# Performance work log

Measured on AMD Instinct MI355X. Metric: run time of the kernel, lower is better.

## Reference

```python
import jax, jax.numpy as jnp
import numpy as np

L = 7          # window side (odd)
A = 0.3        # weight of average term
B = 0.7        # weight of differential term


def mex_hat(d):
    grid = (np.mgrid[:d, :d] - d // 2) * 1.0
    eucl = np.sqrt((grid ** 2).sum(0)) / d
    return (eucl * np.exp(-eucl)).astype(np.float32)  # (d, d)


def setup_inputs() -> dict:
    key = jax.random.key(0)
    x = jax.random.normal(key, (64, 1, 512, 512), dtype=jnp.float32)
    kernel = jnp.asarray(mex_hat(L).reshape(-1))  # (L*L,), matches unfold row-major order
    return {"x": x, "kernel": kernel}


def reference(x, kernel):
    # x: [B,1,n,n], kernel: [L*L]
    n = x.shape[2]
    pad = L // 2
    xp = jnp.pad(x, ((0, 0), (0, 0), (pad, pad), (pad, pad)))  # zero pad, as F.unfold
    mean_acc = jnp.zeros_like(x)
    diff_acc = jnp.zeros_like(x)
    # fixed 49-offset loop replaces the im2col buffer; each shift is a view-slice
    for i in range(L):
        for j in range(L):
            s = jax.lax.dynamic_slice(xp, (0, 0, i, j), x.shape)
            mean_acc = mean_acc + s
            diff_acc = diff_acc + kernel[i * L + j] * jax.nn.relu(s - x)
    average_term = jnp.exp(-mean_acc / (L * L))              # [B,1,n,n]
    differential_term = diff_acc                             # [B,1,n,n]
    mask = A * average_term + B * differential_term
    mask = mask / jnp.sqrt(jnp.sum(mask ** 2))               # global L2 norm
    out = jnp.where(x > mask, x, jnp.zeros_like(x))
    return out, average_term, differential_term
```

## Files before the change

### kernel.cpp

```cpp
#include <hip/hip_runtime.h>
#include <stdint.h>

#define IMG 512
constexpr int TX = 64, TY = 32, PADW = 3;
constexpr int SMW = TX + 2 * PADW;
constexpr int SMH = TY + 2 * PADW;
constexpr int SMS = SMW + 2;
constexpr int NBX = IMG / TX;
constexpr int NBY = IMG / TY;
constexpr float A_W = 0.3f, B_W = 0.7f;

#define W1  0.12383970f
#define W2  0.16507309f
#define W4  0.21470754f
#define W5  0.23209061f
#define W8  0.26975268f
#define W9  0.27918814f
#define W10 0.28754623f
#define W13 0.30773566f
#define W18 0.33061044f

__device__ constexpr float KW[7][7] = {
    { W18, W13, W10, W9,  W10, W13, W18 },
    { W13, W8,  W5,  W4,  W5,  W8,  W13 },
    { W10, W5,  W2,  W1,  W2,  W5,  W10 },
    { W9,  W4,  W1,  0.f, W1,  W4,  W9  },
    { W10, W5,  W2,  W1,  W2,  W5,  W10 },
    { W13, W8,  W5,  W4,  W5,  W8,  W13 },
    { W18, W13, W10, W9,  W10, W13, W18 },
};

constexpr float ksum_calc() {
    float s = 0.f;
    for (int i = 0; i < 7; ++i)
        for (int j = 0; j < 7; ++j) s += KW[i][j];
    return s;
}
constexpr float KSUM = ksum_calc();

__device__ __forceinline__ void stencil8(const float* __restrict__ sm, int tx, int ty0,
                                         float (&avgO)[8], float (&dO)[8])
{
    float c[8], mean[8], T[8];
    #pragma unroll
    for (int k = 0; k < 8; ++k) {
        c[k] = sm[(ty0 + k + PADW) * SMS + tx + PADW];
        mean[k] = 0.f; T[k] = 0.f;
    }

    #pragma unroll
    for (int wy = 0; wy < 14; ++wy) {
        float s[7];
        const int base = (ty0 + wy) * SMS + tx;
        #pragma unroll
        for (int dx = 0; dx < 7; ++dx) s[dx] = sm[base + dx];
        float rowsum = ((s[0] + s[1]) + (s[2] + s[3])) + ((s[4] + s[5]) + s[6]);
        #pragma unroll
        for (int k = 0; k < 8; ++k) {
            const int dy = wy - k;
            if (dy >= 0 && dy < 7) {
                mean[k] += rowsum;
                #pragma unroll
                for (int dx = 0; dx < 7; ++dx) {
                    if (KW[dy][dx] != 0.f)
                        T[k] = fmaf(KW[dy][dx], fmaxf(s[dx], c[k]), T[k]);
                }
            }
        }
    }

    #pragma unroll
    for (int k = 0; k < 8; ++k) {
        avgO[k] = __expf(mean[k] * (-1.f / 49.f));
        dO[k]   = fmaf(-KSUM, c[k], T[k]);
    }
}

__global__ __launch_bounds__(256) void li_pass1(
    const float* __restrict__ x,
    float* __restrict__ outAvg,
    float* __restrict__ outDiff,
    float* __restrict__ partials)
{
    __shared__ float sm[SMH * SMS];
    __shared__ float red[4];
    const int tid = threadIdx.x;

    const int bx = blockIdx.x, by = blockIdx.y, b = blockIdx.z;
    const size_t imgBase = (size_t)b * IMG * IMG;
    const int x0 = bx * TX, y0 = by * TY;

    for (int idx = tid; idx < SMH * SMW; idx += 256) {
        int ly = idx / SMW, lx = idx - ly * SMW;
        int gx = x0 - PADW + lx, gy = y0 - PADW + ly;
        float v = 0.f;
        if ((unsigned)gx < IMG && (unsigned)gy < IMG)
            v = x[imgBase + (size_t)gy * IMG + gx];
        sm[ly * SMS + lx] = v;
    }
    __syncthreads();

    const int tx  = tid & 63;
    const int r   = tid >> 6;
    const int ty0 = r * 8;

    float avgv[8], dv[8];
    stencil8(sm, tx, ty0, avgv, dv);

    float local = 0.f;
    #pragma unroll
    for (int k = 0; k < 8; ++k) {
        float m = fmaf(A_W, avgv[k], B_W * dv[k]);
        local = fmaf(m, m, local);
        size_t g = imgBase + (size_t)(y0 + ty0 + k) * IMG + (x0 + tx);
        outAvg[g]  = avgv[k];
        outDiff[g] = dv[k];
    }

    float v = local;
    #pragma unroll
    for (int off = 32; off > 0; off >>= 1) v += __shfl_down(v, off);
    if ((tid & 63) == 0) red[tid >> 6] = v;
    __syncthreads();
    if (tid == 0) {
        size_t pb = ((size_t)b * gridDim.y + by) * gridDim.x + bx;
        partials[pb] = red[0] + red[1] + red[2] + red[3];
    }
}

__global__ __launch_bounds__(256) void li_pass2(
    const float* __restrict__ partials, int np,
    const float4* __restrict__ x,
    const float4* __restrict__ avg,
    const float4* __restrict__ diff,
    float4* __restrict__ out, long nvec4)
{
    __shared__ float red[4];
    __shared__ float tot_sm;
    const int tid = threadIdx.x;

    float v = 0.f;
    for (int i = tid; i < np; i += 256) v += partials[i];
    #pragma unroll
    for (int off = 32; off > 0; off >>= 1) v += __shfl_down(v, off);
    if ((tid & 63) == 0) red[tid >> 6] = v;
    __syncthreads();
    if (tid == 0) tot_sm = red[0] + red[1] + red[2] + red[3];
    __syncthreads();
    const float inv = 1.0f / sqrtf(tot_sm);

    const size_t stride = (size_t)gridDim.x * 256;
    for (size_t i = (size_t)blockIdx.x * 256 + tid; i < (size_t)nvec4; i += stride) {
        float4 xv = x[i];
        float4 av = avg[i];
        float4 dv = diff[i];
        float4 ov;
        ov.x = (xv.x > fmaf(A_W, av.x, B_W * dv.x) * inv) ? xv.x : 0.f;
        ov.y = (xv.y > fmaf(A_W, av.y, B_W * dv.y) * inv) ? xv.y : 0.f;
        ov.z = (xv.z > fmaf(A_W, av.z, B_W * dv.z) * inv) ? xv.z : 0.f;
        ov.w = (xv.w > fmaf(A_W, av.w, B_W * dv.w) * inv) ? xv.w : 0.f;
        out[i] = ov;
    }
}

extern "C" void kernel_launch(void* const* d_in, const int* in_sizes, int n_in,
                              void* d_out, int out_size, void* d_ws, size_t ws_size,
                              hipStream_t stream)
{
    const float* x = (const float*)d_in[0];
    const int Nelem = in_sizes[0];
    const int batch = Nelem / (IMG * IMG);

    float* out      = (float*)d_out;
    float* outAvg   = out + (size_t)Nelem;
    float* outDiff  = out + (size_t)2 * Nelem;
    float* partials = (float*)d_ws;

    const int np = NBX * NBY * batch;

    dim3 g1(NBX, NBY, batch);
    li_pass1<<<g1, 256, 0, stream>>>(x, outAvg, outDiff, partials);

    const long nvec4 = (long)Nelem / 4;
    li_pass2<<<2048, 256, 0, stream>>>(
        partials, np, (const float4*)x, (const float4*)outAvg,
        (const float4*)outDiff, (float4*)out, nvec4);
}
```

Baseline: 352.1 us.

## Compute two columns per thread and stage mask in output buffer

Each thread now computes two adjacent output columns over a wider 128-column tile. Shared-memory row loads are vectorized as float2 and shared between both columns, and the second row sum is derived from the first by a sliding update. Pass 1 also writes the unnormalized mask into the output buffer, so pass 2 reads x and the mask instead of x, avg and diff, cutting one input stream from the second pass. In exchange the extra mask store adds pass-1 write traffic, and the doubled accumulators increase register pressure.

```diff
diff --git a/kernel.cpp b/kernel.cpp
--- a/kernel.cpp
+++ b/kernel.cpp
@@ -2,13 +2,14 @@
 #include <stdint.h>
 
 #define IMG 512
-constexpr int TX = 64, TY = 32, PADW = 3;
+constexpr float A_W = 0.3f, B_W = 0.7f;
+
+constexpr int TX = 128, TY = 32, PADW = 3;
 constexpr int SMW = TX + 2 * PADW;
 constexpr int SMH = TY + 2 * PADW;
 constexpr int SMS = SMW + 2;
 constexpr int NBX = IMG / TX;
 constexpr int NBY = IMG / TY;
-constexpr float A_W = 0.3f, B_W = 0.7f;
 
 #define W1  0.12383970f
 #define W2  0.16507309f
@@ -38,46 +39,9 @@
 }
 constexpr float KSUM = ksum_calc();
 
-__device__ __forceinline__ void stencil8(const float* __restrict__ sm, int tx, int ty0,
-                                         float (&avgO)[8], float (&dO)[8])
-{
-    float c[8], mean[8], T[8];
-    #pragma unroll
-    for (int k = 0; k < 8; ++k) {
-        c[k] = sm[(ty0 + k + PADW) * SMS + tx + PADW];
-        mean[k] = 0.f; T[k] = 0.f;
-    }
-
-    #pragma unroll
-    for (int wy = 0; wy < 14; ++wy) {
-        float s[7];
-        const int base = (ty0 + wy) * SMS + tx;
-        #pragma unroll
-        for (int dx = 0; dx < 7; ++dx) s[dx] = sm[base + dx];
-        float rowsum = ((s[0] + s[1]) + (s[2] + s[3])) + ((s[4] + s[5]) + s[6]);
-        #pragma unroll
-        for (int k = 0; k < 8; ++k) {
-            const int dy = wy - k;
-            if (dy >= 0 && dy < 7) {
-                mean[k] += rowsum;
-                #pragma unroll
-                for (int dx = 0; dx < 7; ++dx) {
-                    if (KW[dy][dx] != 0.f)
-                        T[k] = fmaf(KW[dy][dx], fmaxf(s[dx], c[k]), T[k]);
-                }
-            }
-        }
-    }
-
-    #pragma unroll
-    for (int k = 0; k < 8; ++k) {
-        avgO[k] = __expf(mean[k] * (-1.f / 49.f));
-        dO[k]   = fmaf(-KSUM, c[k], T[k]);
-    }
-}
-
 __global__ __launch_bounds__(256) void li_pass1(
     const float* __restrict__ x,
+    float* __restrict__ outMask,
     float* __restrict__ outAvg,
     float* __restrict__ outDiff,
     float* __restrict__ partials)
@@ -100,21 +64,59 @@
     }
     __syncthreads();
 
-    const int tx  = tid & 63;
-    const int r   = tid >> 6;
-    const int ty0 = r * 8;
+    const int lane = tid & 63;
+    const int r8   = (tid >> 6) * 8;
+    const int c0   = lane * 2;
 
-    float avgv[8], dv[8];
-    stencil8(sm, tx, ty0, avgv, dv);
+    float cx[8], cy[8], mnx[8], mny[8], Tx[8], Ty[8];
+    #pragma unroll
+    for (int k = 0; k < 8; ++k) {
+        const float* p = &sm[(r8 + k + PADW) * SMS + c0 + PADW];
+        cx[k] = p[0]; cy[k] = p[1];
+        mnx[k] = 0.f; mny[k] = 0.f; Tx[k] = 0.f; Ty[k] = 0.f;
+    }
+
+    #pragma unroll
+    for (int j = 0; j < 14; ++j) {
+        float s[8];
+        const float* row = &sm[(r8 + j) * SMS + c0];
+        #pragma unroll
+        for (int i = 0; i < 4; ++i) {
+            float2 v = *reinterpret_cast<const float2*>(row + 2 * i);
+            s[2 * i] = v.x; s[2 * i + 1] = v.y;
+        }
+        float rs0 = ((s[0] + s[1]) + (s[2] + s[3])) + ((s[4] + s[5]) + s[6]);
+        float rs1 = (rs0 - s[0]) + s[7];
+        #pragma unroll
+        for (int k = 0; k < 8; ++k) {
+            const int dy = j - k;
+            if (dy >= 0 && dy < 7) {
+                mnx[k] += rs0; mny[k] += rs1;
+                #pragma unroll
+                for (int dx = 0; dx < 7; ++dx) {
+                    if (KW[dy][dx] != 0.f) {
+                        Tx[k] = fmaf(KW[dy][dx], fmaxf(s[dx],     cx[k]), Tx[k]);
+                        Ty[k] = fmaf(KW[dy][dx], fmaxf(s[dx + 1], cy[k]), Ty[k]);
+                    }
+                }
+            }
+        }
+    }
 
     float local = 0.f;
     #pragma unroll
     for (int k = 0; k < 8; ++k) {
-        float m = fmaf(A_W, avgv[k], B_W * dv[k]);
-        local = fmaf(m, m, local);
-        size_t g = imgBase + (size_t)(y0 + ty0 + k) * IMG + (x0 + tx);
-        outAvg[g]  = avgv[k];
-        outDiff[g] = dv[k];
+        float ax = __expf(mnx[k] * (-1.f / 49.f));
+        float ay = __expf(mny[k] * (-1.f / 49.f));
+        float dx_ = fmaf(-KSUM, cx[k], Tx[k]);
+        float dy_ = fmaf(-KSUM, cy[k], Ty[k]);
+        float m0 = fmaf(A_W, ax, B_W * dx_);
+        float m1 = fmaf(A_W, ay, B_W * dy_);
+        local = fmaf(m0, m0, fmaf(m1, m1, local));
+        size_t g = imgBase + (size_t)(y0 + r8 + k) * IMG + (x0 + c0);
+        *reinterpret_cast<float2*>(&outAvg[g])  = make_float2(ax, ay);
+        *reinterpret_cast<float2*>(&outDiff[g]) = make_float2(dx_, dy_);
+        *reinterpret_cast<float2*>(&outMask[g]) = make_float2(m0, m1);
     }
 
     float v = local;
@@ -131,9 +133,8 @@
 __global__ __launch_bounds__(256) void li_pass2(
     const float* __restrict__ partials, int np,
     const float4* __restrict__ x,
-    const float4* __restrict__ avg,
-    const float4* __restrict__ diff,
-    float4* __restrict__ out, long nvec4)
+    float4* __restrict__ out,
+    long nvec4)
 {
     __shared__ float red[4];
     __shared__ float tot_sm;
@@ -152,13 +153,12 @@
     const size_t stride = (size_t)gridDim.x * 256;
     for (size_t i = (size_t)blockIdx.x * 256 + tid; i < (size_t)nvec4; i += stride) {
         float4 xv = x[i];
-        float4 av = avg[i];
-        float4 dv = diff[i];
+        float4 mv = out[i];
         float4 ov;
-        ov.x = (xv.x > fmaf(A_W, av.x, B_W * dv.x) * inv) ? xv.x : 0.f;
-        ov.y = (xv.y > fmaf(A_W, av.y, B_W * dv.y) * inv) ? xv.y : 0.f;
-        ov.z = (xv.z > fmaf(A_W, av.z, B_W * dv.z) * inv) ? xv.z : 0.f;
-        ov.w = (xv.w > fmaf(A_W, av.w, B_W * dv.w) * inv) ? xv.w : 0.f;
+        ov.x = (xv.x > mv.x * inv) ? xv.x : 0.f;
+        ov.y = (xv.y > mv.y * inv) ? xv.y : 0.f;
+        ov.z = (xv.z > mv.z * inv) ? xv.z : 0.f;
+        ov.w = (xv.w > mv.w * inv) ? xv.w : 0.f;
         out[i] = ov;
     }
 }
@@ -179,10 +179,9 @@
     const int np = NBX * NBY * batch;
 
     dim3 g1(NBX, NBY, batch);
-    li_pass1<<<g1, 256, 0, stream>>>(x, outAvg, outDiff, partials);
+    li_pass1<<<g1, 256, 0, stream>>>(x, out, outAvg, outDiff, partials);
 
     const long nvec4 = (long)Nelem / 4;
     li_pass2<<<2048, 256, 0, stream>>>(
-        partials, np, (const float4*)x, (const float4*)outAvg,
-        (const float4*)outDiff, (float4*)out, nvec4);
+        partials, np, (const float4*)x, (float4*)out, nvec4);
 }
```

Measured after the change: 350.0 us. No clear change (-0.6%).
